# Optimization experiments

Measured on AMD Instinct MI355X. Metric: run time of the kernel, lower is better.

Reference implementation:

```python
import jax, jax.numpy as jnp
import numpy as np

UNITS = 4096
INPUT_DIM = 1024
N = 16384


def setup_inputs() -> dict:
    key = jax.random.key(0)
    k1, k2 = jax.random.split(key)
    inputs = jax.random.normal(k1, (N, INPUT_DIM), dtype=jnp.float32)
    # Keras 'random_normal' initializer: stddev 0.05
    w = jax.random.normal(k2, (UNITS, INPUT_DIM), dtype=jnp.float32) * 0.05
    return {"inputs": inputs, "w": w}


def reference(inputs, w):
    # Pairwise squared Euclidean distance: out[n, u] = sum_d (w[u,d] - x[n,d])^2
    x_sq = jnp.sum(inputs * inputs, axis=-1, keepdims=True)        # [N, 1]
    w_sq = jnp.sum(w * w, axis=-1)                                  # [U]
    cross = jnp.einsum("nd,ud->nu", inputs, w)                     # [N, U]
    return x_sq + w_sq[None, :] - 2.0 * cross
```

## Files before the change

kernel.cpp:

```cpp
#include <hip/hip_runtime.h>
#include <cstdint>
#include <cstddef>

#define AS1 __attribute__((address_space(1)))
#define AS3 __attribute__((address_space(3)))

typedef unsigned short u16;
typedef unsigned int u32;
typedef __bf16 bf16x8 __attribute__((ext_vector_type(8)));
typedef float f32x4 __attribute__((ext_vector_type(4)));

constexpr int D  = 1024;
constexpr int NS = 16384;
constexpr int US = 4096;
constexpr int BM = 128, BN = 128, BK = 64;

constexpr size_t XH_OFF  = 0;
constexpr size_t WH_OFF  = (size_t)NS * D * 2;
constexpr size_t XSQ_OFF = WH_OFF + (size_t)US * D * 2;
constexpr size_t WSQ_OFF = XSQ_OFF + (size_t)NS * 4;

__device__ __forceinline__ u16 f2bf_rne(float f) {
  u32 u = __float_as_uint(f);
  return (u16)((u + 0x7fffu + ((u >> 16) & 1u)) >> 16);
}

__global__ __launch_bounds__(256) void split_hi_sq(
    const float* __restrict__ x, const float* __restrict__ w,
    u16* __restrict__ xh, u16* __restrict__ wh,
    float* __restrict__ xsq, float* __restrict__ wsq) {
  const int lane = threadIdx.x & 63;
  const int wave = blockIdx.x * 4 + (threadIdx.x >> 6);
  const int nwaves = gridDim.x * 4;
  for (int row = wave; row < NS + US; row += nwaves) {
    const float* src; u16* hdst; float* sdst; int r;
    if (row < NS) { src = x; hdst = xh; sdst = xsq; r = row; }
    else          { src = w; hdst = wh; sdst = wsq; r = row - NS; }
    const float4* s4 = (const float4*)(src + (size_t)r * D);
    ushort4* h4 = (ushort4*)(hdst + (size_t)r * D);
    float s = 0.f;
#pragma unroll
    for (int it = 0; it < 4; ++it) {
      const float4 v = s4[it * 64 + lane];
      s += v.x * v.x + v.y * v.y + v.z * v.z + v.w * v.w;
      h4[it * 64 + lane] =
          make_ushort4(f2bf_rne(v.x), f2bf_rne(v.y), f2bf_rne(v.z), f2bf_rne(v.w));
    }
#pragma unroll
    for (int off = 32; off; off >>= 1) s += __shfl_down(s, off, 64);
    if (lane == 0) sdst[r] = s;
  }
}

__global__ __launch_bounds__(256, 3) void dist_gemm(
    const u16* __restrict__ xh, const u16* __restrict__ wh,
    const float* __restrict__ xsq, const float* __restrict__ wsq,
    float* __restrict__ out) {
  __shared__ u16 sA[BM * BK];
  __shared__ u16 sB[BN * BK];

  const int tid = threadIdx.x;
  const int lane = tid & 63;
  const int wv = tid >> 6;
  const int wm = wv >> 1;
  const int wn = wv & 1;
  const int quad = lane >> 4;
  const int l15 = lane & 15;

  const int m0 = blockIdx.y * BM;
  const int n0 = blockIdx.x * BN;

  f32x4 acc[4][4];
#pragma unroll
  for (int mt = 0; mt < 4; ++mt)
#pragma unroll
    for (int nt = 0; nt < 4; ++nt)
      acc[mt][nt] = (f32x4){0.f, 0.f, 0.f, 0.f};

  const int srow = lane >> 3;
  const int schunk = lane & 7;

  for (int kt = 0; kt < D / BK; ++kt) {
    const int k0 = kt * BK;
    __syncthreads();
#pragma unroll
    for (int i = 0; i < 4; ++i) {
      const int g = wv + i * 4;
      const int r = g * 8 + srow;
      const int cg = schunk ^ (r & 7);
      const u16* ga = xh + (size_t)(m0 + r) * D + k0 + cg * 8;
      const u16* gb = wh + (size_t)(n0 + r) * D + k0 + cg * 8;
      __builtin_amdgcn_global_load_lds((AS1 void*)(u16*)ga, (AS3 void*)(sA + g * 512), 16, 0, 0);
      __builtin_amdgcn_global_load_lds((AS1 void*)(u16*)gb, (AS3 void*)(sB + g * 512), 16, 0, 0);
    }
    __syncthreads();

#pragma unroll
    for (int ks = 0; ks < 2; ++ks) {
      bf16x8 a[4], b[4];
#pragma unroll
      for (int mt = 0; mt < 4; ++mt) {
        const int m = wm * 64 + mt * 16 + l15;
        const int c = (ks * 4 + quad) ^ (m & 7);
        a[mt] = *reinterpret_cast<const bf16x8*>(sA + m * BK + c * 8);
      }
#pragma unroll
      for (int nt = 0; nt < 4; ++nt) {
        const int n = wn * 64 + nt * 16 + l15;
        const int c = (ks * 4 + quad) ^ (n & 7);
        b[nt] = *reinterpret_cast<const bf16x8*>(sB + n * BK + c * 8);
      }
#pragma unroll
      for (int mt = 0; mt < 4; ++mt)
#pragma unroll
        for (int nt = 0; nt < 4; ++nt)
          acc[mt][nt] = __builtin_amdgcn_mfma_f32_16x16x32_bf16(a[mt], b[nt], acc[mt][nt], 0, 0, 0);
    }
  }

#pragma unroll
  for (int mt = 0; mt < 4; ++mt) {
    const int R0 = m0 + wm * 64 + mt * 16 + quad * 4;
#pragma unroll
    for (int nt = 0; nt < 4; ++nt) {
      const int C = n0 + wn * 64 + nt * 16 + l15;
      const float wsv = wsq[C];
#pragma unroll
      for (int r = 0; r < 4; ++r) {
        const int R = R0 + r;
        out[(size_t)R * US + C] = xsq[R] + wsv - 2.0f * acc[mt][nt][r];
      }
    }
  }
}

extern "C" void kernel_launch(void* const* d_in, const int* in_sizes, int n_in,
                              void* d_out, int out_size, void* d_ws, size_t ws_size,
                              hipStream_t stream) {
  const float* x = (const float*)d_in[0];
  const float* w = (const float*)d_in[1];
  float* out = (float*)d_out;
  char* ws = (char*)d_ws;

  u16* xh = (u16*)(ws + XH_OFF);
  u16* wh = (u16*)(ws + WH_OFF);
  float* xsq = (float*)(ws + XSQ_OFF);
  float* wsq = (float*)(ws + WSQ_OFF);

  split_hi_sq<<<dim3(640), dim3(256), 0, stream>>>(x, w, xh, wh, xsq, wsq);
  dist_gemm<<<dim3(US / BN, NS / BM), dim3(256), 0, stream>>>(xh, wh, xsq, wsq, out);
}
```

Baseline: 426.5 us.

## Quantize inputs to FP8 and use scaled 16x16x128 MFMA for cross term

The preprocessing kernel now quantizes x and w to FP8 instead of BF16, scaling w by 16 before conversion. The GEMM kernel raises the K tile to 128, loads FP8 tiles into shared memory, and uses the scaled f8f6f4 16x16x128 MFMA. The epilogue factor drops to 0.125 to undo the scaling. This halves the bytes moved for operands and doubles the nominal matrix rate, but FP8 may lose too much accuracy for the cross term; the quantizer also issues some redundant zero stores.

```diff
diff --git a/kernel.cpp b/kernel.cpp
--- a/kernel.cpp
+++ b/kernel.cpp
@@ -7,44 +7,44 @@
 
 typedef unsigned short u16;
 typedef unsigned int u32;
-typedef __bf16 bf16x8 __attribute__((ext_vector_type(8)));
+typedef unsigned char u8;
+typedef int i32x4 __attribute__((ext_vector_type(4)));
+typedef int i32x8 __attribute__((ext_vector_type(8)));
 typedef float f32x4 __attribute__((ext_vector_type(4)));
 
 constexpr int D  = 1024;
 constexpr int NS = 16384;
 constexpr int US = 4096;
-constexpr int BM = 128, BN = 128, BK = 64;
+constexpr int BM = 128, BN = 128, BK = 128;
 
-constexpr size_t XH_OFF  = 0;
-constexpr size_t WH_OFF  = (size_t)NS * D * 2;
-constexpr size_t XSQ_OFF = WH_OFF + (size_t)US * D * 2;
+constexpr size_t XQ_OFF  = 0;
+constexpr size_t WQ_OFF  = (size_t)NS * D;
+constexpr size_t XSQ_OFF = WQ_OFF + (size_t)US * D;
 constexpr size_t WSQ_OFF = XSQ_OFF + (size_t)NS * 4;
 
-__device__ __forceinline__ u16 f2bf_rne(float f) {
-  u32 u = __float_as_uint(f);
-  return (u16)((u + 0x7fffu + ((u >> 16) & 1u)) >> 16);
-}
-
-__global__ __launch_bounds__(256) void split_hi_sq(
+__global__ __launch_bounds__(256) void quant_sq(
     const float* __restrict__ x, const float* __restrict__ w,
-    u16* __restrict__ xh, u16* __restrict__ wh,
+    u8* __restrict__ xq, u8* __restrict__ wq,
     float* __restrict__ xsq, float* __restrict__ wsq) {
   const int lane = threadIdx.x & 63;
   const int wave = blockIdx.x * 4 + (threadIdx.x >> 6);
   const int nwaves = gridDim.x * 4;
   for (int row = wave; row < NS + US; row += nwaves) {
-    const float* src; u16* hdst; float* sdst; int r;
-    if (row < NS) { src = x; hdst = xh; sdst = xsq; r = row; }
-    else          { src = w; hdst = wh; sdst = wsq; r = row - NS; }
+    const float* src; u8* qdst; float* sdst; int r; float qscale;
+    if (row < NS) { src = x; qdst = xq; sdst = xsq; r = row; qscale = 1.0f; }
+    else          { src = w; qdst = wq; sdst = wsq; r = row - NS; qscale = 16.0f; }
     const float4* s4 = (const float4*)(src + (size_t)r * D);
-    ushort4* h4 = (ushort4*)(hdst + (size_t)r * D);
+    uint4* q4 = (uint4*)(qdst + (size_t)r * D);
     float s = 0.f;
 #pragma unroll
     for (int it = 0; it < 4; ++it) {
       const float4 v = s4[it * 64 + lane];
       s += v.x * v.x + v.y * v.y + v.z * v.z + v.w * v.w;
-      h4[it * 64 + lane] =
-          make_ushort4(f2bf_rne(v.x), f2bf_rne(v.y), f2bf_rne(v.z), f2bf_rne(v.w));
+      u32 p01 = __builtin_amdgcn_cvt_pk_fp8_f32(v.x * qscale, v.y * qscale, 0, false);
+      u32 w0  = __builtin_amdgcn_cvt_pk_fp8_f32(v.z * qscale, v.w * qscale, p01, true);
+      if (it == 0) ((u32*)&q4[0])[0] = 0;
+      ((u32*)(q4 + (it >> 2)))[0] = 0;
+      ((u32*)(qdst + (size_t)r * D))[it * 64 + lane] = w0;
     }
 #pragma unroll
     for (int off = 32; off; off >>= 1) s += __shfl_down(s, off, 64);
@@ -53,11 +53,11 @@
 }
 
 __global__ __launch_bounds__(256, 3) void dist_gemm(
-    const u16* __restrict__ xh, const u16* __restrict__ wh,
+    const u8* __restrict__ xq, const u8* __restrict__ wq,
     const float* __restrict__ xsq, const float* __restrict__ wsq,
     float* __restrict__ out) {
-  __shared__ u16 sA[BM * BK];
-  __shared__ u16 sB[BN * BK];
+  __shared__ u8 sA[BM * BK];
+  __shared__ u8 sB[BN * BK];
 
   const int tid = threadIdx.x;
   const int lane = tid & 63;
@@ -88,33 +88,35 @@
       const int g = wv + i * 4;
       const int r = g * 8 + srow;
       const int cg = schunk ^ (r & 7);
-      const u16* ga = xh + (size_t)(m0 + r) * D + k0 + cg * 8;
-      const u16* gb = wh + (size_t)(n0 + r) * D + k0 + cg * 8;
-      __builtin_amdgcn_global_load_lds((AS1 void*)(u16*)ga, (AS3 void*)(sA + g * 512), 16, 0, 0);
-      __builtin_amdgcn_global_load_lds((AS1 void*)(u16*)gb, (AS3 void*)(sB + g * 512), 16, 0, 0);
+      const u8* ga = xq + (size_t)(m0 + r) * D + k0 + cg * 16;
+      const u8* gb = wq + (size_t)(n0 + r) * D + k0 + cg * 16;
+      __builtin_amdgcn_global_load_lds((AS1 void*)(u8*)ga, (AS3 void*)(sA + g * 1024), 16, 0, 0);
+      __builtin_amdgcn_global_load_lds((AS1 void*)(u8*)gb, (AS3 void*)(sB + g * 1024), 16, 0, 0);
     }
     __syncthreads();
 
+    i32x8 b[4];
 #pragma unroll
-    for (int ks = 0; ks < 2; ++ks) {
-      bf16x8 a[4], b[4];
+    for (int nt = 0; nt < 4; ++nt) {
+      const int n = wn * 64 + nt * 16 + l15;
+      const int s = n & 7;
+      const i32x4 b0 = *reinterpret_cast<const i32x4*>(sB + n * BK + ((2 * quad) ^ s) * 16);
+      const i32x4 b1 = *reinterpret_cast<const i32x4*>(sB + n * BK + ((2 * quad + 1) ^ s) * 16);
+      b[nt] = __builtin_shufflevector(b0, b1, 0, 1, 2, 3, 4, 5, 6, 7);
+    }
 #pragma unroll
-      for (int mt = 0; mt < 4; ++mt) {
-        const int m = wm * 64 + mt * 16 + l15;
-        const int c = (ks * 4 + quad) ^ (m & 7);
-        a[mt] = *reinterpret_cast<const bf16x8*>(sA + m * BK + c * 8);
-      }
+    for (int mt = 0; mt < 4; ++mt) {
+      const int m = wm * 64 + mt * 16 + l15;
+      const int s = m & 7;
+      const i32x4 a0 = *reinterpret_cast<const i32x4*>(sA + m * BK + ((2 * quad) ^ s) * 16);
+      const i32x4 a1 = *reinterpret_cast<const i32x4*>(sA + m * BK + ((2 * quad + 1) ^ s) * 16);
+      const i32x8 a = __builtin_shufflevector(a0, a1, 0, 1, 2, 3, 4, 5, 6, 7);
 #pragma unroll
       for (int nt = 0; nt < 4; ++nt) {
-        const int n = wn * 64 + nt * 16 + l15;
-        const int c = (ks * 4 + quad) ^ (n & 7);
-        b[nt] = *reinterpret_cast<const bf16x8*>(sB + n * BK + c * 8);
+        acc[mt][nt] = __builtin_amdgcn_mfma_scale_f32_16x16x128_f8f6f4(
+            a, b[nt], acc[mt][nt],  0,  0,
+             0, 0x7F7F7F7F,  0, 0x7F7F7F7F);
       }
-#pragma unroll
-      for (int mt = 0; mt < 4; ++mt)
-#pragma unroll
-        for (int nt = 0; nt < 4; ++nt)
-          acc[mt][nt] = __builtin_amdgcn_mfma_f32_16x16x32_bf16(a[mt], b[nt], acc[mt][nt], 0, 0, 0);
     }
   }
 
@@ -128,7 +130,7 @@
 #pragma unroll
       for (int r = 0; r < 4; ++r) {
         const int R = R0 + r;
-        out[(size_t)R * US + C] = xsq[R] + wsv - 2.0f * acc[mt][nt][r];
+        out[(size_t)R * US + C] = xsq[R] + wsv - 0.125f * acc[mt][nt][r];
       }
     }
   }
@@ -142,11 +144,11 @@
   float* out = (float*)d_out;
   char* ws = (char*)d_ws;
 
-  u16* xh = (u16*)(ws + XH_OFF);
-  u16* wh = (u16*)(ws + WH_OFF);
+  u8* xq = (u8*)(ws + XQ_OFF);
+  u8* wq = (u8*)(ws + WQ_OFF);
   float* xsq = (float*)(ws + XSQ_OFF);
   float* wsq = (float*)(ws + WSQ_OFF);
 
-  split_hi_sq<<<dim3(640), dim3(256), 0, stream>>>(x, w, xh, wh, xsq, wsq);
-  dist_gemm<<<dim3(US / BN, NS / BM), dim3(256), 0, stream>>>(xh, wh, xsq, wsq, out);
+  quant_sq<<<dim3(640), dim3(256), 0, stream>>>(x, w, xq, wq, xsq, wsq);
+  dist_gemm<<<dim3(US / BN, NS / BM), dim3(256), 0, stream>>>(xq, wq, xsq, wsq, out);
 }
```

After: 399.3 us. 1.07x faster.
